# Kernel optimization log

Measured on AMD Instinct MI355X. Metric: run time of the kernel, lower is better.

## Reference

```python
import jax, jax.numpy as jnp
import numpy as np

N_VARS = 1_000_000
NB, NS, NL = 400_000, 300_000, 200_000  # binary / small-int / large-int counts
C_CLS = 16
N_CON = 500_000
E = 16_000_000
LP_SOL_COL = 8
BIAS_COL = 1
LAMBDA_MEAN, LAMBDA_MAX = 1.0, 0.1


def setup_inputs() -> dict:
    key = jax.random.key(0)
    ks = jax.random.split(key, 10)
    # disjoint variable index partitions: [0,NB) bin, [NB,NB+NS) small int,
    # [NB+NS,NB+NS+NL) large int, rest continuous (var_types==0)
    idx_bin = jnp.arange(NB, dtype=jnp.int64)
    idx_int_small = jnp.arange(NB, NB + NS, dtype=jnp.int64)
    idx_int_large = jnp.arange(NB + NS, NB + NS + NL, dtype=jnp.int64)
    var_types = jnp.concatenate([
        jnp.ones(NB, dtype=jnp.int64),                 # binary
        jnp.full((NS + NL,), 2, dtype=jnp.int64),      # integer
        jnp.zeros(N_VARS - NB - NS - NL, dtype=jnp.int64),  # continuous
    ])
    edge_indices = jnp.stack([
        jax.random.randint(ks[0], (E,), 0, N_CON, dtype=jnp.int64),
        jax.random.randint(ks[1], (E,), 0, N_VARS, dtype=jnp.int64),
    ])
    return {
        'prob_bin': jax.random.uniform(ks[2], (NB, 1), jnp.float32),
        'logits_int_small': jax.random.normal(ks[3], (NS, C_CLS), jnp.float32),
        'int_small_offsets': jax.random.normal(ks[4], (NS,), jnp.float32),
        'pred_int_large': jax.random.normal(ks[5], (NL, 1), jnp.float32),
        'edge_features': jax.random.normal(ks[6], (E, 1), jnp.float32),
        'constraint_features': jax.random.normal(ks[7], (N_CON, 8), jnp.float32),
        'variable_features': jax.random.normal(ks[8], (N_VARS, 16), jnp.float32),
        'idx_bin': idx_bin,
        'idx_int_small': idx_int_small,
        'idx_int_large': idx_int_large,
        'var_types': var_types,
        'edge_indices': edge_indices,
        'n_vars': N_VARS,
    }


def _build_x(prob_bin, logits_int_small, int_small_offsets, pred_int_large,
             variable_features, idx_bin, idx_int_small, idx_int_large,
             var_types, n_vars):
    x = jnp.zeros((n_vars,), dtype=prob_bin.dtype)
    x = x.at[idx_bin].set(prob_bin[:, 0])
    # expected value of small-int class distribution
    probs = jax.nn.softmax(logits_int_small, axis=-1)                  # [NS, C]
    class_values = jnp.arange(logits_int_small.shape[1], dtype=probs.dtype)
    expected = probs @ class_values + int_small_offsets                # [NS]
    x = x.at[idx_int_small].set(expected)
    x = x.at[idx_int_large].set(pred_int_large[:, 0])
    # continuous vars take detached LP solution values
    lp_vals = jax.lax.stop_gradient(variable_features[:, LP_SOL_COL])
    x = jnp.where(var_types == 0, lp_vals, x)
    return x


def reference(prob_bin, logits_int_small, int_small_offsets, pred_int_large,
              edge_features, constraint_features, variable_features,
              idx_bin, idx_int_small, idx_int_large, var_types,
              edge_indices, n_vars):
    x = _build_x(prob_bin, logits_int_small, int_small_offsets, pred_int_large,
                 variable_features, idx_bin, idx_int_small, idx_int_large,
                 var_types, n_vars)
    n_cons = constraint_features.shape[0]
    # sparse A @ x: gather variable values along edges, scale, scatter-add per constraint
    weighted = edge_features.reshape(-1) * x[edge_indices[1]]          # [E]
    Ax = jax.ops.segment_sum(weighted, edge_indices[0], num_segments=n_cons)
    violation = jax.nn.relu(Ax - constraint_features[:, BIAS_COL])     # [N_con]
    mean_viol = violation.mean()
    max_viol = violation.max()
    n_violated = jnp.sum(violation > 1e-6)
    penalty = LAMBDA_MEAN * mean_viol + LAMBDA_MAX * max_viol
    return penalty, mean_viol, max_viol, n_violated
```

## Files before the change

kernel.cpp:

```cpp
#include <hip/hip_runtime.h>


#define BSHIFT 14
#define BROWS  (1 << BSHIFT)
#define NBUCK_MAX 32
#define CHUNK 8192
#define ROUNDS (CHUNK / 1024)
#define BUF 128
#define THRESH 48
#define SPLIT 16

typedef int      iv4 __attribute__((ext_vector_type(4)));
typedef float    fv4 __attribute__((ext_vector_type(4)));
typedef unsigned uv2 __attribute__((ext_vector_type(2)));
typedef unsigned uv4 __attribute__((ext_vector_type(4)));

__device__ inline unsigned bf16bits(float v) {
    unsigned f = __float_as_uint(v);
    return (f + 0x7FFFu + ((f >> 16) & 1u)) >> 16;
}


__global__ __launch_bounds__(256) void k_build_x(
    const float* __restrict__ prob_bin, const int* __restrict__ idx_bin, int NB, int gBin,
    const float* __restrict__ logits, const float* __restrict__ offs,
    const int* __restrict__ idx_small, int NS, int gSml,
    const float* __restrict__ pred, const int* __restrict__ idx_large, int NL, int gLrg,
    const int* __restrict__ vt, const float* __restrict__ vf, int NV,
    float* __restrict__ x, float* __restrict__ acc)
{
    int blk = blockIdx.x, tid = threadIdx.x;
    if (blk == 0 && tid < 4) reinterpret_cast<unsigned*>(acc)[tid] = 0u;

    if (blk < gBin) {
        int i = blk * 256 + tid;
        if (i < NB) x[idx_bin[i]] = prob_bin[i];
        return;
    }
    blk -= gBin;
    if (blk < gSml) {
        int i = blk * 256 + tid;
        if (i < NS) {
            const fv4* lp = reinterpret_cast<const fv4*>(logits + (size_t)i * 16);
            fv4 v0 = lp[0], v1 = lp[1], v2 = lp[2], v3 = lp[3];
            float l[16] = {v0.x, v0.y, v0.z, v0.w, v1.x, v1.y, v1.z, v1.w,
                           v2.x, v2.y, v2.z, v2.w, v3.x, v3.y, v3.z, v3.w};
            float m = l[0];
#pragma unroll
            for (int j = 1; j < 16; ++j) m = fmaxf(m, l[j]);
            float s = 0.f, ws = 0.f;
#pragma unroll
            for (int j = 0; j < 16; ++j) {
                float e = expf(l[j] - m);
                s += e;
                ws += e * (float)j;
            }
            x[idx_small[i]] = ws / s + offs[i];
        }
        return;
    }
    blk -= gSml;
    if (blk < gLrg) {
        int i = blk * 256 + tid;
        if (i < NL) x[idx_large[i]] = pred[i];
        return;
    }
    blk -= gLrg;
    {
        int v = blk * 256 + tid;
        if (v < NV && vt[v] == 0) x[v] = vf[(size_t)v * 16 + 8];
    }
}


template <bool PROD>
__global__ __launch_bounds__(256) void k_hist_prod(const int* __restrict__ rows,
                                                   const int* __restrict__ cols,
                                                   const float* __restrict__ ef,
                                                   const float* __restrict__ x,
                                                   int* __restrict__ counts,
                                                   unsigned* __restrict__ prods,
                                                   int nchunks, int E, int nbuck) {
    __shared__ int h[4][NBUCK_MAX];
    int tid = threadIdx.x, chunk = blockIdx.x, wid = tid >> 6, lane = tid & 63;
    if (lane < NBUCK_MAX) h[wid][lane] = 0;
    __syncthreads();
    int e4max = E >> 2;
    int b4 = chunk * (CHUNK / 4);
#pragma unroll
    for (int k = 0; k < ROUNDS; ++k) {
        int i4 = b4 + k * 256 + tid;
        if (i4 < e4max) {
            iv4 r = __builtin_nontemporal_load(reinterpret_cast<const iv4*>(rows) + i4);
            atomicAdd(&h[wid][r.x >> BSHIFT], 1);
            atomicAdd(&h[wid][r.y >> BSHIFT], 1);
            atomicAdd(&h[wid][r.z >> BSHIFT], 1);
            atomicAdd(&h[wid][r.w >> BSHIFT], 1);
            if (PROD) {
                iv4 c = __builtin_nontemporal_load(reinterpret_cast<const iv4*>(cols) + i4);
                fv4 f = __builtin_nontemporal_load(reinterpret_cast<const fv4*>(ef) + i4);
                unsigned p01 = bf16bits(f.x * x[c.x]) | (bf16bits(f.y * x[c.y]) << 16);
                unsigned p23 = bf16bits(f.z * x[c.z]) | (bf16bits(f.w * x[c.w]) << 16);
                uv2 p = {p01, p23};
                __builtin_nontemporal_store(p, reinterpret_cast<uv2*>(prods) + i4);
            }
        }
    }
    if (chunk == 0 && tid < (E & 3)) {
        int e = (E & ~3) + tid;
        atomicAdd(&h[wid][rows[e] >> BSHIFT], 1);
        if (PROD)
            reinterpret_cast<unsigned short*>(prods)[e] =
                (unsigned short)bf16bits(ef[e] * x[cols[e]]);
    }
    __syncthreads();
    if (tid < nbuck)
        counts[(size_t)tid * nchunks + chunk] = h[0][tid] + h[1][tid] + h[2][tid] + h[3][tid];
}


__global__ __launch_bounds__(1024) void k_scan(const int* __restrict__ counts,
                                               int* __restrict__ off,
                                               int* __restrict__ total, int nchunks) {
    int b = blockIdx.x;
    __shared__ int wtot[16];
    __shared__ int wbase[16];
    int tid = threadIdx.x, w = tid >> 6, lane = tid & 63;
    int seg = (nchunks + 15) >> 4;
    int lo = w * seg;
    int hi = lo + seg; if (hi > nchunks) hi = nchunks;
    const int* cb = counts + (size_t)b * nchunks;
    int* ob = off + (size_t)b * nchunks;
    int carry = 0;
    for (int i0 = lo; i0 < hi; i0 += 64) {
        int i = i0 + lane;
        int v = (i < hi) ? cb[i] : 0;
        int orig = v;
#pragma unroll
        for (int o = 1; o < 64; o <<= 1) {
            int t = __shfl_up(v, o, 64);
            if (lane >= o) v += t;
        }
        if (i < hi) ob[i] = carry + v - orig;
        carry += __shfl(v, 63, 64);
    }
    if (lane == 0) wtot[w] = carry;
    __syncthreads();
    if (tid == 0) {
        int s = 0;
        for (int k = 0; k < 16; ++k) { wbase[k] = s; s += wtot[k]; }
        total[b] = s;
    }
    __syncthreads();
    int add = wbase[w];
    if (add)
        for (int i = lo + lane; i < hi; i += 64) ob[i] += add;
}


template <bool PROD>
__global__ __launch_bounds__(256) void k_scatter5(const int* __restrict__ rows,
                                                  const int* __restrict__ cols,
                                                  const float* __restrict__ ef,
                                                  const float* __restrict__ x,
                                                  const unsigned* __restrict__ prods,
                                                  const int* __restrict__ off,
                                                  const int* __restrict__ total,
                                                  unsigned* __restrict__ recs,
                                                  int nchunks, int E, int nbuck) {
    __shared__ unsigned bufr[NBUCK_MAX][BUF];
    __shared__ int fill[NBUCK_MAX];
    __shared__ int done[NBUCK_MAX];
    __shared__ int cbase[NBUCK_MAX];

    int tid = threadIdx.x, chunk = blockIdx.x, wid = tid >> 6, lane = tid & 63;
    if (tid < 32) {
        int t = (tid < nbuck) ? total[tid] : 0;
        int p = (t + 3) & ~3;
        int sc = p;
#pragma unroll
        for (int o = 1; o < 32; o <<= 1) {
            int u = __shfl_up(sc, o, 64);
            if (tid >= o) sc += u;
        }
        cbase[tid] = (sc - p) + ((tid < nbuck) ? off[(size_t)tid * nchunks + chunk] : 0);
        fill[tid] = 0;
        done[tid] = 0;
    }
    __syncthreads();

    int e4max = E >> 2;
    int b4 = chunk * (CHUNK / 4);

    iv4 r, c; fv4 f; uv2 p; bool v;
#define LOADK(k)                                                              \
    {   int i4 = b4 + (k) * 256 + tid;                                        \
        v = i4 < e4max;                                                       \
        if (v) {                                                              \
            r = __builtin_nontemporal_load(reinterpret_cast<const iv4*>(rows) + i4); \
            if (PROD) {                                                       \
                p = __builtin_nontemporal_load(reinterpret_cast<const uv2*>(prods) + i4); \
            } else {                                                          \
                c = __builtin_nontemporal_load(reinterpret_cast<const iv4*>(cols) + i4); \
                f = __builtin_nontemporal_load(reinterpret_cast<const fv4*>(ef) + i4);   \
            }                                                                 \
        } }

    LOADK(0)
    for (int k = 0; k < ROUNDS; ++k) {
        iv4 rr = r; iv4 cc = c; fv4 ff = f; uv2 pp = p; bool vv = v;
        if (k + 1 < ROUNDS) LOADK(k + 1)
        if (vv) {
            unsigned q[4];
            if (PROD) {
                q[0] = pp.x & 0xFFFFu; q[1] = pp.x >> 16;
                q[2] = pp.y & 0xFFFFu; q[3] = pp.y >> 16;
            } else {
                q[0] = bf16bits(ff.x * x[cc.x]);
                q[1] = bf16bits(ff.y * x[cc.y]);
                q[2] = bf16bits(ff.z * x[cc.z]);
                q[3] = bf16bits(ff.w * x[cc.w]);
            }
            int ra[4] = {rr.x, rr.y, rr.z, rr.w};
#pragma unroll
            for (int j = 0; j < 4; ++j) {
                int b = ra[j] >> BSHIFT;
                unsigned rec = ((unsigned)(ra[j] & (BROWS - 1)) << 16) | q[j];
                int pos = atomicAdd(&fill[b], 1);
                if (pos < BUF) bufr[b][pos] = rec;
                else recs[cbase[b] + done[b] + pos] = rec;
            }
        }
        if (k == ROUNDS - 1 && chunk == 0 && tid < (E & 3)) {
            int e = (E & ~3) + tid;
            int rrow = rows[e];
            unsigned q16 = PROD ? (unsigned)reinterpret_cast<const unsigned short*>(prods)[e]
                                : bf16bits(ef[e] * x[cols[e]]);
            int b = rrow >> BSHIFT;
            unsigned rec = ((unsigned)(rrow & (BROWS - 1)) << 16) | q16;
            int pos = atomicAdd(&fill[b], 1);
            if (pos < BUF) bufr[b][pos] = rec;
            else recs[cbase[b] + done[b] + pos] = rec;
        }
        __syncthreads();
        bool last = (k == ROUNDS - 1);
        for (int b = wid; b < nbuck; b += 4) {
            int fl = fill[b];
            if (fl == 0) continue;
            if (fl >= THRESH || last) {
                int n = fl < BUF ? fl : BUF;
                int g = cbase[b] + done[b];
                for (int j = lane; j < n; j += 64) recs[g + j] = bufr[b][j];
                if (lane == 0) { done[b] += fl; fill[b] = 0; }
            }
        }
        __syncthreads();
    }
#undef LOADK
}


__global__ __launch_bounds__(256) void k_accum(const unsigned* __restrict__ recs,
                                               const int* __restrict__ total,
                                               float* __restrict__ partial, int nbuck) {
    __shared__ float tile[BROWS];
    __shared__ int sb[2];
    int tid = threadIdx.x;
    int b = blockIdx.x / SPLIT, s = blockIdx.x % SPLIT;
    if (tid < 32) {
        int t = (tid < nbuck) ? total[tid] : 0;
        int pq = (t + 3) & ~3;
        int sc = pq;
#pragma unroll
        for (int o = 1; o < 32; o <<= 1) {
            int u = __shfl_up(sc, o, 64);
            if (tid >= o) sc += u;
        }
        if (tid == b) { sb[0] = sc - pq; sb[1] = t; }
    }
    fv4 z = {0.f, 0.f, 0.f, 0.f};
    for (int i = tid; i < BROWS / 4; i += 256) reinterpret_cast<fv4*>(tile)[i] = z;
    __syncthreads();
    int lo = sb[0], len = sb[1], hi = lo + len;
    int per = ((len + SPLIT - 1) / SPLIT + 3) & ~3;
    int s0 = lo + s * per;
    int s1 = s0 + per; if (s1 > hi) s1 = hi;
    int i = s0 + (tid << 2);
    for (; i + 3 < s1; i += 1024) {
        uv4 r = __builtin_nontemporal_load(reinterpret_cast<const uv4*>(recs + i));
        atomicAdd(&tile[r.x >> 16], __uint_as_float((r.x & 0xFFFFu) << 16));
        atomicAdd(&tile[r.y >> 16], __uint_as_float((r.y & 0xFFFFu) << 16));
        atomicAdd(&tile[r.z >> 16], __uint_as_float((r.z & 0xFFFFu) << 16));
        atomicAdd(&tile[r.w >> 16], __uint_as_float((r.w & 0xFFFFu) << 16));
    }
    if (i < s1)
        for (int j = i; j < s1; ++j) {
            unsigned rr = recs[j];
            atomicAdd(&tile[rr >> 16], __uint_as_float((rr & 0xFFFFu) << 16));
        }
    __syncthreads();
    float* out = partial + ((size_t)blockIdx.x << BSHIFT);
    for (int j = tid; j < BROWS / 4; j += 256)
        __builtin_nontemporal_store(reinterpret_cast<const fv4*>(tile)[j],
                                    reinterpret_cast<fv4*>(out) + j);
}


__global__ __launch_bounds__(256) void k_reduce_fin(const float* __restrict__ partial,
                                                    const float* __restrict__ cf,
                                                    float* __restrict__ acc,
                                                    float* __restrict__ out,
                                                    int ncon, int nblocks) {
    float lsum = 0.f, lmax = 0.f;
    unsigned lcnt = 0;
    int stride = gridDim.x * blockDim.x;
    for (int c = blockIdx.x * blockDim.x + threadIdx.x; c < ncon; c += stride) {
        int b = c >> BSHIFT, i = c & (BROWS - 1);
        const float* p = partial + (((size_t)b * SPLIT) << BSHIFT) + i;
        float v = 0.f;
#pragma unroll
        for (int s = 0; s < SPLIT; ++s)
            v += __builtin_nontemporal_load(p + ((size_t)s << BSHIFT));
        v -= cf[(size_t)c * 8 + 1];
        v = v > 0.f ? v : 0.f;
        lsum += v;
        lmax = fmaxf(lmax, v);
        lcnt += (v > 1e-6f) ? 1u : 0u;
    }
#pragma unroll
    for (int o = 32; o > 0; o >>= 1) {
        lsum += __shfl_down(lsum, o);
        lmax = fmaxf(lmax, __shfl_down(lmax, o));
        lcnt += __shfl_down(lcnt, o);
    }
    __shared__ float ssum[4];
    __shared__ float smax[4];
    __shared__ unsigned scnt[4];
    int lane = threadIdx.x & 63, wid = threadIdx.x >> 6;
    if (lane == 0) { ssum[wid] = lsum; smax[wid] = lmax; scnt[wid] = lcnt; }
    __syncthreads();
    if (threadIdx.x == 0) {
        float bs = 0.f, bm = 0.f;
        unsigned bc = 0;
        for (int w = 0; w < 4; ++w) { bs += ssum[w]; bm = fmaxf(bm, smax[w]); bc += scnt[w]; }
        atomicAdd(&acc[0], bs);
        atomicMax(reinterpret_cast<unsigned*>(acc) + 1, __float_as_uint(bm));
        atomicAdd(reinterpret_cast<unsigned*>(acc) + 2, bc);
        __threadfence();
        unsigned t = atomicAdd(reinterpret_cast<unsigned*>(acc) + 3, 1u);
        if (t == (unsigned)(nblocks - 1)) {
            float sum   = atomicAdd(&acc[0], 0.f);
            unsigned mb = atomicMax(reinterpret_cast<unsigned*>(acc) + 1, 0u);
            unsigned ct = atomicAdd(reinterpret_cast<unsigned*>(acc) + 2, 0u);
            float mean = sum / (float)ncon;
            float mx = __uint_as_float(mb);
            out[0] = mean + 0.1f * mx;
            out[1] = mean;
            out[2] = mx;
            out[3] = (float)ct;
        }
    }
}


__global__ void k_edges(const float* __restrict__ ef, const int* __restrict__ rows,
                        const int* __restrict__ cols, const float* __restrict__ x,
                        float* __restrict__ Ax, int e4, int E) {
    int stride = gridDim.x * blockDim.x;
    int gid = blockIdx.x * blockDim.x + threadIdx.x;
    for (int i = gid; i < e4; i += stride) {
        fv4 f = reinterpret_cast<const fv4*>(ef)[i];
        iv4 r = reinterpret_cast<const iv4*>(rows)[i];
        iv4 c = reinterpret_cast<const iv4*>(cols)[i];
        atomicAdd(&Ax[r.x], f.x * x[c.x]);
        atomicAdd(&Ax[r.y], f.y * x[c.y]);
        atomicAdd(&Ax[r.z], f.z * x[c.z]);
        atomicAdd(&Ax[r.w], f.w * x[c.w]);
    }
    for (int e = e4 * 4 + gid; e < E; e += stride)
        atomicAdd(&Ax[rows[e]], ef[e] * x[cols[e]]);
}

__global__ void k_reduce_ax(const float* __restrict__ Ax, const float* __restrict__ cf,
                            float* __restrict__ acc, float* __restrict__ out,
                            int ncon, int nblocks) {
    float lsum = 0.f, lmax = 0.f;
    unsigned lcnt = 0;
    int stride = gridDim.x * blockDim.x;
    for (int c = blockIdx.x * blockDim.x + threadIdx.x; c < ncon; c += stride) {
        float v = Ax[c] - cf[(size_t)c * 8 + 1];
        v = v > 0.f ? v : 0.f;
        lsum += v;
        lmax = fmaxf(lmax, v);
        lcnt += (v > 1e-6f) ? 1u : 0u;
    }
#pragma unroll
    for (int o = 32; o > 0; o >>= 1) {
        lsum += __shfl_down(lsum, o);
        lmax = fmaxf(lmax, __shfl_down(lmax, o));
        lcnt += __shfl_down(lcnt, o);
    }
    __shared__ float ssum[4];
    __shared__ float smax[4];
    __shared__ unsigned scnt[4];
    int lane = threadIdx.x & 63, wid = threadIdx.x >> 6;
    if (lane == 0) { ssum[wid] = lsum; smax[wid] = lmax; scnt[wid] = lcnt; }
    __syncthreads();
    if (threadIdx.x == 0) {
        float bs = 0.f, bm = 0.f;
        unsigned bc = 0;
        for (int w = 0; w < 4; ++w) { bs += ssum[w]; bm = fmaxf(bm, smax[w]); bc += scnt[w]; }
        atomicAdd(&acc[0], bs);
        atomicMax(reinterpret_cast<unsigned*>(acc) + 1, __float_as_uint(bm));
        atomicAdd(reinterpret_cast<unsigned*>(acc) + 2, bc);
        __threadfence();
        unsigned t = atomicAdd(reinterpret_cast<unsigned*>(acc) + 3, 1u);
        if (t == (unsigned)(nblocks - 1)) {
            float sum   = atomicAdd(&acc[0], 0.f);
            unsigned mb = atomicMax(reinterpret_cast<unsigned*>(acc) + 1, 0u);
            unsigned ct = atomicAdd(reinterpret_cast<unsigned*>(acc) + 2, 0u);
            float mean = sum / (float)ncon;
            float mx = __uint_as_float(mb);
            out[0] = mean + 0.1f * mx;
            out[1] = mean;
            out[2] = mx;
            out[3] = (float)ct;
        }
    }
}


extern "C" void kernel_launch(void* const* d_in, const int* in_sizes, int n_in,
                              void* d_out, int out_size, void* d_ws, size_t ws_size,
                              hipStream_t stream) {
    const float* prob_bin     = (const float*)d_in[0];
    const float* logits_small = (const float*)d_in[1];
    const float* offs_small   = (const float*)d_in[2];
    const float* pred_large   = (const float*)d_in[3];
    const float* edge_feat    = (const float*)d_in[4];
    const float* cons_feat    = (const float*)d_in[5];
    const float* var_feat     = (const float*)d_in[6];
    const int*   idx_bin      = (const int*)d_in[7];
    const int*   idx_small    = (const int*)d_in[8];
    const int*   idx_large    = (const int*)d_in[9];
    const int*   var_types    = (const int*)d_in[10];
    const int*   edge_indices = (const int*)d_in[11];

    const int NB    = in_sizes[0];
    const int NS    = in_sizes[2];
    const int NL    = in_sizes[3];
    const int E     = in_sizes[4];
    const int NCON  = in_sizes[5] / 8;
    const int NVARS = in_sizes[10];

    const int* rows = edge_indices;
    const int* cols = edge_indices + E;

    const int nbuck   = (NCON + BROWS - 1) >> BSHIFT;
    const int nchunks = (E + CHUNK - 1) / CHUNK;

    char* w = (char*)d_ws;
    size_t o = 0;
    auto take = [&](size_t bytes) -> char* {
        char* p = w + o;
        o = (o + bytes + 255) & ~(size_t)255;
        return p;
    };
    float*    x       = (float*)take((size_t)NVARS * 4);
    unsigned* recs    = (unsigned*)take((size_t)(E + 4 * NBUCK_MAX) * 4);
    float*    partial = (float*)take((size_t)nbuck * SPLIT * BROWS * 4);
    int*      counts  = (int*)take((size_t)nbuck * nchunks * 4);
    int*      off     = (int*)take((size_t)nbuck * nchunks * 4);
    int*      total   = (int*)take((size_t)nbuck * 4);
    float*    acc     = (float*)take(32);
    size_t needB = o;
    unsigned* prods   = (unsigned*)take((size_t)(E / 2 + 8) * 4);
    size_t needA = o;

    const int B = 256;
    bool tierA = (ws_size >= needA) && (nbuck <= NBUCK_MAX);
    bool tierB = (ws_size >= needB) && (nbuck <= NBUCK_MAX);

    if (tierA || tierB) {
        const int gBin = (NB + B - 1) / B;
        const int gSml = (NS + B - 1) / B;
        const int gLrg = (NL + B - 1) / B;
        const int gCnt = (NVARS + B - 1) / B;

        k_build_x<<<gBin + gSml + gLrg + gCnt, B, 0, stream>>>(
            prob_bin, idx_bin, NB, gBin,
            logits_small, offs_small, idx_small, NS, gSml,
            pred_large, idx_large, NL, gLrg,
            var_types, var_feat, NVARS, x, acc);

        if (tierA)
            k_hist_prod<true><<<nchunks, B, 0, stream>>>(rows, cols, edge_feat, x,
                                                         counts, prods, nchunks, E, nbuck);
        else
            k_hist_prod<false><<<nchunks, B, 0, stream>>>(rows, cols, edge_feat, x,
                                                          counts, prods, nchunks, E, nbuck);

        k_scan<<<nbuck, 1024, 0, stream>>>(counts, off, total, nchunks);

        if (tierA)
            k_scatter5<true><<<nchunks, B, 0, stream>>>(rows, cols, edge_feat, x, prods,
                                                        off, total, recs, nchunks, E, nbuck);
        else
            k_scatter5<false><<<nchunks, B, 0, stream>>>(rows, cols, edge_feat, x, prods,
                                                         off, total, recs, nchunks, E, nbuck);

        k_accum<<<nbuck * SPLIT, B, 0, stream>>>(recs, total, partial, nbuck);
        const int rblocks = 1024;
        k_reduce_fin<<<rblocks, B, 0, stream>>>(partial, cons_feat, acc, (float*)d_out,
                                                NCON, rblocks);
    } else {
        float* accf = (float*)((char*)d_ws + (size_t)NVARS * 4);
        float* Ax   = accf + 8;
        (void)hipMemsetAsync(accf, 0, (size_t)(8 + NCON) * sizeof(float), stream);
        const int gBin = (NB + B - 1) / B;
        const int gSml = (NS + B - 1) / B;
        const int gLrg = (NL + B - 1) / B;
        const int gCnt = (NVARS + B - 1) / B;
        k_build_x<<<gBin + gSml + gLrg + gCnt, B, 0, stream>>>(
            prob_bin, idx_bin, NB, gBin,
            logits_small, offs_small, idx_small, NS, gSml,
            pred_large, idx_large, NL, gLrg,
            var_types, var_feat, NVARS, x, accf);
        k_edges<<<2048, B, 0, stream>>>(edge_feat, rows, cols, x, Ax, E / 4, E);
        k_reduce_ax<<<1024, B, 0, stream>>>(Ax, cons_feat, accf, (float*)d_out, NCON, 1024);
    }
}
```

Baseline: 314.7 us.

## Store x as bf16, fuse histogram into build, gather in scatter directly

```diff
diff --git a/kernel.cpp b/kernel.cpp
--- a/kernel.cpp
+++ b/kernel.cpp
@@ -8,33 +8,63 @@
 #define ROUNDS (CHUNK / 1024)
 #define BUF 128
 #define THRESH 48
-#define SPLIT 16
+#define SPLIT 8
 
 typedef int      iv4 __attribute__((ext_vector_type(4)));
 typedef float    fv4 __attribute__((ext_vector_type(4)));
-typedef unsigned uv2 __attribute__((ext_vector_type(2)));
 typedef unsigned uv4 __attribute__((ext_vector_type(4)));
 
 __device__ inline unsigned bf16bits(float v) {
     unsigned f = __float_as_uint(v);
     return (f + 0x7FFFu + ((f >> 16) & 1u)) >> 16;
 }
-
-
-__global__ __launch_bounds__(256) void k_build_x(
+__device__ inline float bf16val(unsigned bits) {
+    return __uint_as_float(bits << 16);
+}
+
+
+__global__ __launch_bounds__(256) void k_build_hist(
+    const int* __restrict__ rows, int* __restrict__ counts, int nchunks, int gHist,
     const float* __restrict__ prob_bin, const int* __restrict__ idx_bin, int NB, int gBin,
     const float* __restrict__ logits, const float* __restrict__ offs,
     const int* __restrict__ idx_small, int NS, int gSml,
     const float* __restrict__ pred, const int* __restrict__ idx_large, int NL, int gLrg,
     const int* __restrict__ vt, const float* __restrict__ vf, int NV,
-    float* __restrict__ x, float* __restrict__ acc)
+    int E, int nbuck, unsigned short* __restrict__ xb, float* __restrict__ acc)
 {
     int blk = blockIdx.x, tid = threadIdx.x;
     if (blk == 0 && tid < 4) reinterpret_cast<unsigned*>(acc)[tid] = 0u;
 
+    if (blk < gHist) {
+        __shared__ int h[4][NBUCK_MAX];
+        int wid = tid >> 6, lane = tid & 63;
+        if (lane < NBUCK_MAX) h[wid][lane] = 0;
+        __syncthreads();
+        int e4max = E >> 2;
+        int b4 = blk * (CHUNK / 4);
+#pragma unroll
+        for (int k = 0; k < ROUNDS; ++k) {
+            int i4 = b4 + k * 256 + tid;
+            if (i4 < e4max) {
+                iv4 r = __builtin_nontemporal_load(reinterpret_cast<const iv4*>(rows) + i4);
+                atomicAdd(&h[wid][r.x >> BSHIFT], 1);
+                atomicAdd(&h[wid][r.y >> BSHIFT], 1);
+                atomicAdd(&h[wid][r.z >> BSHIFT], 1);
+                atomicAdd(&h[wid][r.w >> BSHIFT], 1);
+            }
+        }
+        if (blk == 0 && tid < (E & 3))
+            atomicAdd(&h[wid][rows[(E & ~3) + tid] >> BSHIFT], 1);
+        __syncthreads();
+        if (tid < nbuck)
+            counts[(size_t)tid * nchunks + blk] =
+                h[0][tid] + h[1][tid] + h[2][tid] + h[3][tid];
+        return;
+    }
+    blk -= gHist;
     if (blk < gBin) {
         int i = blk * 256 + tid;
-        if (i < NB) x[idx_bin[i]] = prob_bin[i];
+        if (i < NB) xb[idx_bin[i]] = (unsigned short)bf16bits(prob_bin[i]);
         return;
     }
     blk -= gBin;
@@ -55,67 +85,21 @@
                 s += e;
                 ws += e * (float)j;
             }
-            x[idx_small[i]] = ws / s + offs[i];
+            xb[idx_small[i]] = (unsigned short)bf16bits(ws / s + offs[i]);
         }
         return;
     }
     blk -= gSml;
     if (blk < gLrg) {
         int i = blk * 256 + tid;
-        if (i < NL) x[idx_large[i]] = pred[i];
+        if (i < NL) xb[idx_large[i]] = (unsigned short)bf16bits(pred[i]);
         return;
     }
     blk -= gLrg;
     {
         int v = blk * 256 + tid;
-        if (v < NV && vt[v] == 0) x[v] = vf[(size_t)v * 16 + 8];
-    }
-}
-
-
-template <bool PROD>
-__global__ __launch_bounds__(256) void k_hist_prod(const int* __restrict__ rows,
-                                                   const int* __restrict__ cols,
-                                                   const float* __restrict__ ef,
-                                                   const float* __restrict__ x,
-                                                   int* __restrict__ counts,
-                                                   unsigned* __restrict__ prods,
-                                                   int nchunks, int E, int nbuck) {
-    __shared__ int h[4][NBUCK_MAX];
-    int tid = threadIdx.x, chunk = blockIdx.x, wid = tid >> 6, lane = tid & 63;
-    if (lane < NBUCK_MAX) h[wid][lane] = 0;
-    __syncthreads();
-    int e4max = E >> 2;
-    int b4 = chunk * (CHUNK / 4);
-#pragma unroll
-    for (int k = 0; k < ROUNDS; ++k) {
-        int i4 = b4 + k * 256 + tid;
-        if (i4 < e4max) {
-            iv4 r = __builtin_nontemporal_load(reinterpret_cast<const iv4*>(rows) + i4);
-            atomicAdd(&h[wid][r.x >> BSHIFT], 1);
-            atomicAdd(&h[wid][r.y >> BSHIFT], 1);
-            atomicAdd(&h[wid][r.z >> BSHIFT], 1);
-            atomicAdd(&h[wid][r.w >> BSHIFT], 1);
-            if (PROD) {
-                iv4 c = __builtin_nontemporal_load(reinterpret_cast<const iv4*>(cols) + i4);
-                fv4 f = __builtin_nontemporal_load(reinterpret_cast<const fv4*>(ef) + i4);
-                unsigned p01 = bf16bits(f.x * x[c.x]) | (bf16bits(f.y * x[c.y]) << 16);
-                unsigned p23 = bf16bits(f.z * x[c.z]) | (bf16bits(f.w * x[c.w]) << 16);
-                uv2 p = {p01, p23};
-                __builtin_nontemporal_store(p, reinterpret_cast<uv2*>(prods) + i4);
-            }
-        }
-    }
-    if (chunk == 0 && tid < (E & 3)) {
-        int e = (E & ~3) + tid;
-        atomicAdd(&h[wid][rows[e] >> BSHIFT], 1);
-        if (PROD)
-            reinterpret_cast<unsigned short*>(prods)[e] =
-                (unsigned short)bf16bits(ef[e] * x[cols[e]]);
-    }
-    __syncthreads();
-    if (tid < nbuck)
-        counts[(size_t)tid * nchunks + chunk] = h[0][tid] + h[1][tid] + h[2][tid] + h[3][tid];
+        if (v < NV && vt[v] == 0) xb[v] = (unsigned short)bf16bits(vf[(size_t)v * 16 + 8]);
+    }
 }
 
 
@@ -158,12 +142,10 @@
 }
 
 
-template <bool PROD>
-__global__ __launch_bounds__(256) void k_scatter5(const int* __restrict__ rows,
+__global__ __launch_bounds__(256) void k_scatter6(const int* __restrict__ rows,
                                                   const int* __restrict__ cols,
                                                   const float* __restrict__ ef,
-                                                  const float* __restrict__ x,
-                                                  const unsigned* __restrict__ prods,
+                                                  const unsigned short* __restrict__ xb,
                                                   const int* __restrict__ off,
                                                   const int* __restrict__ total,
                                                   unsigned* __restrict__ recs,
@@ -192,36 +174,35 @@
     int e4max = E >> 2;
     int b4 = chunk * (CHUNK / 4);
 
-    iv4 r, c; fv4 f; uv2 p; bool v;
-#define LOADK(k)                                                              \
-    {   int i4 = b4 + (k) * 256 + tid;                                        \
-        v = i4 < e4max;                                                       \
-        if (v) {                                                              \
-            r = __builtin_nontemporal_load(reinterpret_cast<const iv4*>(rows) + i4); \
-            if (PROD) {                                                       \
-                p = __builtin_nontemporal_load(reinterpret_cast<const uv2*>(prods) + i4); \
-            } else {                                                          \
-                c = __builtin_nontemporal_load(reinterpret_cast<const iv4*>(cols) + i4); \
-                f = __builtin_nontemporal_load(reinterpret_cast<const fv4*>(ef) + i4);   \
-            }                                                                 \
+    iv4 rA, cA; fv4 fA; bool vA;
+    iv4 rB, cB; fv4 fB; bool vB;
+    unsigned gA0, gA1, gA2, gA3, gB0, gB1, gB2, gB3;
+
+#define LOADK(k, R, C, F, V)                                                   \
+    {   int i4 = b4 + (k) * 256 + tid;                                         \
+        V = i4 < e4max;                                                        \
+        if (V) {                                                               \
+            R = __builtin_nontemporal_load(reinterpret_cast<const iv4*>(rows) + i4); \
+            C = __builtin_nontemporal_load(reinterpret_cast<const iv4*>(cols) + i4); \
+            F = __builtin_nontemporal_load(reinterpret_cast<const fv4*>(ef) + i4);   \
         } }
-
-    LOADK(0)
+#define GATHK(C, V, G0, G1, G2, G3)                                            \
+    if (V) { G0 = xb[C.x]; G1 = xb[C.y]; G2 = xb[C.z]; G3 = xb[C.w]; }
+
+    LOADK(0, rA, cA, fA, vA)
+    GATHK(cA, vA, gA0, gA1, gA2, gA3)
+
     for (int k = 0; k < ROUNDS; ++k) {
-        iv4 rr = r; iv4 cc = c; fv4 ff = f; uv2 pp = p; bool vv = v;
-        if (k + 1 < ROUNDS) LOADK(k + 1)
-        if (vv) {
-            unsigned q[4];
-            if (PROD) {
-                q[0] = pp.x & 0xFFFFu; q[1] = pp.x >> 16;
-                q[2] = pp.y & 0xFFFFu; q[3] = pp.y >> 16;
-            } else {
-                q[0] = bf16bits(ff.x * x[cc.x]);
-                q[1] = bf16bits(ff.y * x[cc.y]);
-                q[2] = bf16bits(ff.z * x[cc.z]);
-                q[3] = bf16bits(ff.w * x[cc.w]);
-            }
-            int ra[4] = {rr.x, rr.y, rr.z, rr.w};
+        if (k + 1 < ROUNDS) {
+            LOADK(k + 1, rB, cB, fB, vB)
+            GATHK(cB, vB, gB0, gB1, gB2, gB3)
+        }
+        if (vA) {
+            unsigned q[4] = {bf16bits(fA.x * bf16val(gA0)),
+                             bf16bits(fA.y * bf16val(gA1)),
+                             bf16bits(fA.z * bf16val(gA2)),
+                             bf16bits(fA.w * bf16val(gA3))};
+            int ra[4] = {rA.x, rA.y, rA.z, rA.w};
 #pragma unroll
             for (int j = 0; j < 4; ++j) {
                 int b = ra[j] >> BSHIFT;
@@ -234,10 +215,9 @@
         if (k == ROUNDS - 1 && chunk == 0 && tid < (E & 3)) {
             int e = (E & ~3) + tid;
             int rrow = rows[e];
-            unsigned q16 = PROD ? (unsigned)reinterpret_cast<const unsigned short*>(prods)[e]
-                                : bf16bits(ef[e] * x[cols[e]]);
+            unsigned rec = ((unsigned)(rrow & (BROWS - 1)) << 16)
+                         | bf16bits(ef[e] * bf16val(xb[cols[e]]));
             int b = rrow >> BSHIFT;
-            unsigned rec = ((unsigned)(rrow & (BROWS - 1)) << 16) | q16;
             int pos = atomicAdd(&fill[b], 1);
             if (pos < BUF) bufr[b][pos] = rec;
             else recs[cbase[b] + done[b] + pos] = rec;
@@ -250,13 +230,17 @@
             if (fl >= THRESH || last) {
                 int n = fl < BUF ? fl : BUF;
                 int g = cbase[b] + done[b];
-                for (int j = lane; j < n; j += 64) recs[g + j] = bufr[b][j];
+                for (int j = lane; j < n; j += 64)
+                    __builtin_nontemporal_store(bufr[b][j], recs + g + j);
                 if (lane == 0) { done[b] += fl; fill[b] = 0; }
             }
         }
         __syncthreads();
+        rA = rB; cA = cB; fA = fB; vA = vB;
+        gA0 = gB0; gA1 = gB1; gA2 = gB2; gA3 = gB3;
     }
 #undef LOADK
+#undef GATHK
 }
 
 
@@ -364,7 +348,7 @@
 
 
 __global__ void k_edges(const float* __restrict__ ef, const int* __restrict__ rows,
-                        const int* __restrict__ cols, const float* __restrict__ x,
+                        const int* __restrict__ cols, const unsigned short* __restrict__ xb,
                         float* __restrict__ Ax, int e4, int E) {
     int stride = gridDim.x * blockDim.x;
     int gid = blockIdx.x * blockDim.x + threadIdx.x;
@@ -372,13 +356,13 @@
         fv4 f = reinterpret_cast<const fv4*>(ef)[i];
         iv4 r = reinterpret_cast<const iv4*>(rows)[i];
         iv4 c = reinterpret_cast<const iv4*>(cols)[i];
-        atomicAdd(&Ax[r.x], f.x * x[c.x]);
-        atomicAdd(&Ax[r.y], f.y * x[c.y]);
-        atomicAdd(&Ax[r.z], f.z * x[c.z]);
-        atomicAdd(&Ax[r.w], f.w * x[c.w]);
+        atomicAdd(&Ax[r.x], f.x * bf16val(xb[c.x]));
+        atomicAdd(&Ax[r.y], f.y * bf16val(xb[c.y]));
+        atomicAdd(&Ax[r.z], f.z * bf16val(xb[c.z]));
+        atomicAdd(&Ax[r.w], f.w * bf16val(xb[c.w]));
     }
     for (int e = e4 * 4 + gid; e < E; e += stride)
-        atomicAdd(&Ax[rows[e]], ef[e] * x[cols[e]]);
+        atomicAdd(&Ax[rows[e]], ef[e] * bf16val(xb[cols[e]]));
 }
 
 __global__ void k_reduce_ax(const float* __restrict__ Ax, const float* __restrict__ cf,
@@ -466,67 +450,50 @@
         o = (o + bytes + 255) & ~(size_t)255;
         return p;
     };
-    float*    x       = (float*)take((size_t)NVARS * 4);
-    unsigned* recs    = (unsigned*)take((size_t)(E + 4 * NBUCK_MAX) * 4);
-    float*    partial = (float*)take((size_t)nbuck * SPLIT * BROWS * 4);
-    int*      counts  = (int*)take((size_t)nbuck * nchunks * 4);
-    int*      off     = (int*)take((size_t)nbuck * nchunks * 4);
-    int*      total   = (int*)take((size_t)nbuck * 4);
-    float*    acc     = (float*)take(32);
-    size_t needB = o;
-    unsigned* prods   = (unsigned*)take((size_t)(E / 2 + 8) * 4);
-    size_t needA = o;
+    unsigned short* xb = (unsigned short*)take((size_t)NVARS * 2);
+    unsigned* recs     = (unsigned*)take((size_t)(E + 4 * NBUCK_MAX) * 4);
+    float*    partial  = (float*)take((size_t)nbuck * SPLIT * BROWS * 4);
+    int*      counts   = (int*)take((size_t)nbuck * nchunks * 4);
+    int*      off      = (int*)take((size_t)nbuck * nchunks * 4);
+    int*      total    = (int*)take((size_t)nbuck * 4);
+    float*    acc      = (float*)take(32);
+    size_t need = o;
 
     const int B = 256;
-    bool tierA = (ws_size >= needA) && (nbuck <= NBUCK_MAX);
-    bool tierB = (ws_size >= needB) && (nbuck <= NBUCK_MAX);
-
-    if (tierA || tierB) {
-        const int gBin = (NB + B - 1) / B;
-        const int gSml = (NS + B - 1) / B;
-        const int gLrg = (NL + B - 1) / B;
-        const int gCnt = (NVARS + B - 1) / B;
-
-        k_build_x<<<gBin + gSml + gLrg + gCnt, B, 0, stream>>>(
+    bool sorted_path = (ws_size >= need) && (nbuck <= NBUCK_MAX);
+
+    const int gBin = (NB + B - 1) / B;
+    const int gSml = (NS + B - 1) / B;
+    const int gLrg = (NL + B - 1) / B;
+    const int gCnt = (NVARS + B - 1) / B;
+
+    if (sorted_path) {
+        k_build_hist<<<nchunks + gBin + gSml + gLrg + gCnt, B, 0, stream>>>(
+            rows, counts, nchunks, nchunks,
             prob_bin, idx_bin, NB, gBin,
             logits_small, offs_small, idx_small, NS, gSml,
             pred_large, idx_large, NL, gLrg,
-            var_types, var_feat, NVARS, x, acc);
-
-        if (tierA)
-            k_hist_prod<true><<<nchunks, B, 0, stream>>>(rows, cols, edge_feat, x,
-                                                         counts, prods, nchunks, E, nbuck);
-        else
-            k_hist_prod<false><<<nchunks, B, 0, stream>>>(rows, cols, edge_feat, x,
-                                                          counts, prods, nchunks, E, nbuck);
-
+            var_types, var_feat, NVARS,
+            E, nbuck, xb, acc);
         k_scan<<<nbuck, 1024, 0, stream>>>(counts, off, total, nchunks);
-
-        if (tierA)
-            k_scatter5<true><<<nchunks, B, 0, stream>>>(rows, cols, edge_feat, x, prods,
-                                                        off, total, recs, nchunks, E, nbuck);
-        else
-            k_scatter5<false><<<nchunks, B, 0, stream>>>(rows, cols, edge_feat, x, prods,
-                                                         off, total, recs, nchunks, E, nbuck);
-
+        k_scatter6<<<nchunks, B, 0, stream>>>(rows, cols, edge_feat, xb, off, total,
+                                              recs, nchunks, E, nbuck);
         k_accum<<<nbuck * SPLIT, B, 0, stream>>>(recs, total, partial, nbuck);
         const int rblocks = 1024;
         k_reduce_fin<<<rblocks, B, 0, stream>>>(partial, cons_feat, acc, (float*)d_out,
                                                 NCON, rblocks);
     } else {
-        float* accf = (float*)((char*)d_ws + (size_t)NVARS * 4);
+        float* accf = (float*)((char*)d_ws + (((size_t)NVARS * 2 + 255) & ~(size_t)255));
         float* Ax   = accf + 8;
         (void)hipMemsetAsync(accf, 0, (size_t)(8 + NCON) * sizeof(float), stream);
-        const int gBin = (NB + B - 1) / B;
-        const int gSml = (NS + B - 1) / B;
-        const int gLrg = (NL + B - 1) / B;
-        const int gCnt = (NVARS + B - 1) / B;
-        k_build_x<<<gBin + gSml + gLrg + gCnt, B, 0, stream>>>(
+        k_build_hist<<<gBin + gSml + gLrg + gCnt, B, 0, stream>>>(
+            rows, counts, nchunks, 0,
             prob_bin, idx_bin, NB, gBin,
             logits_small, offs_small, idx_small, NS, gSml,
             pred_large, idx_large, NL, gLrg,
-            var_types, var_feat, NVARS, x, accf);
-        k_edges<<<2048, B, 0, stream>>>(edge_feat, rows, cols, x, Ax, E / 4, E);
+            var_types, var_feat, NVARS,
+            E, nbuck, xb, accf);
+        k_edges<<<2048, B, 0, stream>>>(edge_feat, rows, cols, xb, Ax, E / 4, E);
         k_reduce_ax<<<1024, B, 0, stream>>>(Ax, cons_feat, accf, (float*)d_out, NCON, 1024);
     }
 }
```

After: 274.5 us (median of 2 runs). -12.8%, faster.
